# Kernel optimization log

Measured on AMD Instinct MI355X. Metric: run time of the kernel, lower is better.

## Reference

```python
import jax, jax.numpy as jnp
import numpy as np

N_NODES = 50000
N_EDGES = 1_600_000
IN_DIM = 128
HID = 32
HEADS = 4
NEG_SLOPE = 0.2


def setup_inputs() -> dict:
    key = jax.random.key(0)
    ks = jax.random.split(key, 6)
    h = jax.random.normal(ks[0], (N_NODES, IN_DIM), dtype=jnp.float32)
    src = jax.random.randint(ks[1], (N_EDGES,), 0, N_NODES, dtype=jnp.int32)
    dst = jax.random.randint(ks[2], (N_EDGES,), 0, N_NODES, dtype=jnp.int32)
    s = 1.0 / np.sqrt(IN_DIM)  # ~ Linear default init scale
    Wq = (jax.random.normal(ks[3], (HEADS, IN_DIM, HID), dtype=jnp.float32) * s)
    Wk = (jax.random.normal(ks[4], (HEADS, IN_DIM, HID), dtype=jnp.float32) * s)
    Wv = (jax.random.normal(ks[5], (HEADS, IN_DIM, HID), dtype=jnp.float32) * s)
    return {"h": h, "src": src, "dst": dst, "Wq": Wq, "Wk": Wk, "Wv": Wv}


def _gat_forward(h, src, dst, Wq, Wk, Wv):
    n = h.shape[0]
    # per-head projections: [H, N, D]
    q = jnp.einsum('ni,hio->hno', h, Wq)
    k = jnp.einsum('ni,hio->hno', h, Wk)
    v = jnp.einsum('ni,hio->hno', h, Wv)
    # edge scores: e = leaky_relu(<q_src, k_dst>)  -> [H, E]
    e = jax.nn.leaky_relu(jnp.einsum('hed,hed->he', q[:, src], k[:, dst]),
                          negative_slope=NEG_SLOPE)
    # segment softmax over incoming edges of each dst node
    seg_max = jax.vmap(lambda x: jax.ops.segment_max(x, dst, num_segments=n))(e)
    seg_max = jax.lax.stop_gradient(jnp.where(jnp.isfinite(seg_max), seg_max, 0.0))
    ex = jnp.exp(e - seg_max[:, dst])                       # [H, E]
    denom = jax.vmap(lambda x: jax.ops.segment_sum(x, dst, num_segments=n))(ex)
    alpha = ex / jnp.maximum(denom, 1e-9)[:, dst]           # [H, E]
    # weighted scatter-sum of source values into dst nodes: [H, N, D]
    msg = alpha[..., None] * v[:, src]
    out = jax.vmap(lambda m: jax.ops.segment_sum(m, dst, num_segments=n))(msg)
    # concat heads along feature dim -> [N, H*D]
    return out.transpose(1, 0, 2).reshape(n, HEADS * HID)


def reference(h, src, dst, Wq, Wk, Wv):
    return _gat_forward(h, src, dst, Wq, Wk, Wv)
```

## Files before the change

### kernel.cpp

```cpp
#include <hip/hip_runtime.h>
#include <hip/hip_fp16.h>

#define IN_DIM 128
#define HID 32
#define HEADS 4
#define OUTC (HEADS*HID)
#define NEG_SLOPE 0.2f
#define BSH 4
#define BN 16
#define BCAP 768
#define NBMAX 3200
#define NCOLS 384
#define WPB 192
#define NP 25
#define PSH 11
#define PCAP 72704
#define PBLK 18

typedef _Float16 f16x8 __attribute__((ext_vector_type(8)));
typedef float    f32x4 __attribute__((ext_vector_type(4)));

__device__ __forceinline__ unsigned short f2h(float f) {
    return __half_as_ushort(__float2half_rn(f));
}
__device__ __forceinline__ float2 h2f2(unsigned u) {
    __half2 h = *reinterpret_cast<__half2*>(&u);
    return __half22float2(h);
}
__device__ __forceinline__ float qdot2(const uint2& w, const float4& kd) {
    float2 a = h2f2(w.x);
    float2 b = h2f2(w.y);
    return a.x * kd.x + a.y * kd.y + b.x * kd.z + b.y * kd.w;
}
__device__ __forceinline__ void vacc2(const uint2& w, float e, float4& acc) {
    float2 a = h2f2(w.x);
    float2 b = h2f2(w.y);
    acc.x = fmaf(e, a.x, acc.x);
    acc.y = fmaf(e, a.y, acc.y);
    acc.z = fmaf(e, b.x, acc.z);
    acc.w = fmaf(e, b.y, acc.w);
}

__global__ __launch_bounds__(256) void w_prep(
    const float* __restrict__ Wq, const float* __restrict__ Wk,
    const float* __restrict__ Wv, unsigned short* __restrict__ Wt,
    int* __restrict__ gcount, int* __restrict__ pcount)
{
    int idx = blockIdx.x * 256 + threadIdx.x;
    if (idx < NBMAX) gcount[idx] = 0;
    if (idx >= NBMAX && idx < NBMAX + NP) pcount[idx - NBMAX] = 0;
    if (idx >= NCOLS * IN_DIM) return;
    int c = idx >> 7, k = idx & 127;
    int sel = c >> 7;
    int cc  = c & 127;
    int head = cc >> 5, dcol = cc & 31;
    const float* W = (sel == 0) ? Wk : (sel == 1) ? Wq : Wv;
    Wt[idx] = f2h(W[(size_t)head * IN_DIM * HID + (size_t)k * HID + dcol]);
}

__global__ __launch_bounds__(256) void part_proj(
    const int* __restrict__ src, const int* __restrict__ dst,
    int* __restrict__ pcount, unsigned* __restrict__ ppairs,
    const float* __restrict__ h, const unsigned short* __restrict__ Wt,
    unsigned short* __restrict__ K, unsigned short* __restrict__ Qa,
    unsigned short* __restrict__ Va,
    int ne, int binblk, int n)
{
    __shared__ __align__(16) char smem_raw[32 * IN_DIM * 2];
    const int tid = threadIdx.x;

    if ((int)blockIdx.x < binblk) {
        int* hist = (int*)smem_raw;
        int* base = hist + 32;
        const int bblk = blockIdx.x;

        if (tid < 32) hist[tid] = 0;
        __syncthreads();

        const int ne4 = ne >> 2;
        const int4* s4 = (const int4*)src;
        const int4* d4 = (const int4*)dst;

        int4 sv[4], dv[4];
        int loc[16], pk[16];
        bool val[4];
#pragma unroll
        for (int k2 = 0; k2 < 4; ++k2) {
            int idx = bblk * 1024 + k2 * 256 + tid;
            val[k2] = idx < ne4;
            if (val[k2]) { sv[k2] = s4[idx]; dv[k2] = d4[idx]; }
            else { sv[k2] = make_int4(0,0,0,0); dv[k2] = make_int4(0,0,0,0); }
        }
#pragma unroll
        for (int k2 = 0; k2 < 4; ++k2) {
            int dd[4] = { dv[k2].x, dv[k2].y, dv[k2].z, dv[k2].w };
#pragma unroll
            for (int j = 0; j < 4; ++j) {
                int p = dd[j] >> PSH;
                pk[k2*4+j]  = p;
                loc[k2*4+j] = val[k2] ? atomicAdd(&hist[p], 1) : 0;
            }
        }
        __syncthreads();
        if (tid < 32) base[tid] = hist[tid] ? atomicAdd(&pcount[tid], hist[tid]) : 0;
        __syncthreads();
#pragma unroll
        for (int k2 = 0; k2 < 4; ++k2) {
            if (!val[k2]) continue;
            int ss[4] = { sv[k2].x, sv[k2].y, sv[k2].z, sv[k2].w };
            int dd[4] = { dv[k2].x, dv[k2].y, dv[k2].z, dv[k2].w };
#pragma unroll
            for (int j = 0; j < 4; ++j) {
                int p   = pk[k2*4+j];
                int pos = base[p] + loc[k2*4+j];
                if (pos < PCAP)
                    ppairs[(size_t)p * PCAP + pos] =
                        ((unsigned)ss[j] << 16) | (unsigned)dd[j];
            }
        }
        if (bblk == 0 && tid == 0) {
            for (int e = ne4 * 4; e < ne; ++e) {
                int p   = dst[e] >> PSH;
                int pos = atomicAdd(&pcount[p], 1);
                if (pos < PCAP)
                    ppairs[(size_t)p * PCAP + pos] =
                        ((unsigned)src[e] << 16) | (unsigned)dst[e];
            }
        }
        return;
    }

    unsigned short* hsm = (unsigned short*)smem_raw;
    const int row0 = (blockIdx.x - binblk) * 32;

    for (int idx = tid; idx < 32 * 64; idx += 256) {
        int r  = idx >> 6;
        int c2 = idx & 63;
        int gr = row0 + r;
        float2 hv = (gr < n) ? ((const float2*)h)[(size_t)gr * 64 + c2]
                             : make_float2(0.f, 0.f);
        int col = c2 * 2;
        int sc  = col ^ ((r & 7) << 3);
        __half2 packed = __floats2half2_rn(hv.x, hv.y);
        *(unsigned*)&hsm[r * IN_DIM + sc] = *(unsigned*)&packed;
    }
    __syncthreads();

    const int w = tid >> 6;
    const int l = tid & 63;
    const int l15 = l & 15;
    const int kg  = l >> 4;
    const _Float16* Wt16 = (const _Float16*)Wt;

    f32x4 acc[2][6];
#pragma unroll
    for (int rt = 0; rt < 2; ++rt)
#pragma unroll
        for (int ct = 0; ct < 6; ++ct) acc[rt][ct] = (f32x4){0.f, 0.f, 0.f, 0.f};

#pragma unroll
    for (int s = 0; s < 4; ++s) {
        int scol = (s * 32 + kg * 8) ^ ((l & 7) << 3);
        f16x8 a0 = *(const f16x8*)&hsm[l15 * IN_DIM + scol];
        f16x8 a1 = *(const f16x8*)&hsm[(l15 + 16) * IN_DIM + scol];
#pragma unroll
        for (int ct = 0; ct < 6; ++ct) {
            int c = w * 96 + ct * 16 + l15;
            f16x8 b = *(const f16x8*)&Wt16[(size_t)c * IN_DIM + s * 32 + kg * 8];
            acc[0][ct] = __builtin_amdgcn_mfma_f32_16x16x32_f16(a0, b, acc[0][ct], 0, 0, 0);
            acc[1][ct] = __builtin_amdgcn_mfma_f32_16x16x32_f16(a1, b, acc[1][ct], 0, 0, 0);
        }
    }

#pragma unroll
    for (int rt = 0; rt < 2; ++rt) {
#pragma unroll
        for (int ct = 0; ct < 6; ++ct) {
            int cD = w * 96 + ct * 16 + l15;
#pragma unroll
            for (int r = 0; r < 4; ++r) {
                int node = row0 + rt * 16 + kg * 4 + r;
                if (node >= n) continue;
                unsigned short hv = f2h(acc[rt][ct][r]);
                if (cD < 128) {
                    K[(size_t)node * OUTC + cD] = hv;
                } else if (cD < 256) {
                    Qa[(size_t)node * OUTC + (cD - 128)] = hv;
                } else {
                    Va[(size_t)node * OUTC + (cD - 256)] = hv;
                }
            }
        }
    }
}

__global__ __launch_bounds__(256) void pass2(
    const unsigned* __restrict__ ppairs, const int* __restrict__ pcount,
    int* __restrict__ gcount, unsigned* __restrict__ pairs)
{
    __shared__ int hist[128], base[128];
    const int p   = blockIdx.x / PBLK;
    const int c   = blockIdx.x % PBLK;
    const int tid = threadIdx.x;

    int mp = pcount[p]; if (mp > PCAP) mp = PCAP;
    const int i0 = c * 4096;
    if (i0 >= mp) return;
    const int iend = min(i0 + 4096, mp);

    if (tid < 128) hist[tid] = 0;
    __syncthreads();

    const unsigned* pp = ppairs + (size_t)p * PCAP;
    unsigned rec[16];
    int loc[16], lb[16];
#pragma unroll
    for (int k = 0; k < 16; ++k) {
        int i = i0 + k * 256 + tid;
        if (i < iend) {
            unsigned r = pp[i];
            rec[k] = r;
            int b = ((r & 0xFFFFu) >> BSH) & 127;
            lb[k]  = b;
            loc[k] = atomicAdd(&hist[b], 1);
        } else {
            rec[k] = 0; lb[k] = -1; loc[k] = 0;
        }
    }
    __syncthreads();
    if (tid < 128) base[tid] = hist[tid] ? atomicAdd(&gcount[p * 128 + tid], hist[tid]) : 0;
    __syncthreads();
#pragma unroll
    for (int k = 0; k < 16; ++k) {
        if (lb[k] < 0) continue;
        unsigned r = rec[k];
        int gb  = p * 128 + lb[k];
        int pos = base[lb[k]] + loc[k];
        if (pos < BCAP)
            pairs[(size_t)gb * BCAP + pos] =
                ((r >> 16) << BSH) | (r & (BN - 1));
    }
}

__global__ __launch_bounds__(256) void gat_bucket(
    const unsigned* __restrict__ pairs, const int* __restrict__ gcount,
    const uint2* __restrict__ Q2, const uint2* __restrict__ V2,
    const ushort4* __restrict__ K4,
    float* __restrict__ out, int n, int nbuck)
{
    __shared__ unsigned short sl[BCAP];
    __shared__ float exls[BCAP * 4];
    __shared__ int cl[BN], cur[BN], off[BN + 1];

    const int b = blockIdx.x;
    if (b >= nbuck) return;
    const int tid = threadIdx.x;

    if (tid < BN) cl[tid] = 0;
    __syncthreads();

    int m = gcount[b]; if (m > BCAP) m = BCAP;
    const unsigned* pb = pairs + (size_t)b * BCAP;

    for (int i = tid; i < m; i += 256) atomicAdd(&cl[pb[i] & (BN - 1)], 1);
    __syncthreads();
    if (tid == 0) {
        int a = 0;
#pragma unroll
        for (int i = 0; i < BN; ++i) { off[i] = a; cur[i] = a; a += cl[i]; }
        off[BN] = a;
    }
    __syncthreads();
    for (int i = tid; i < m; i += 256) {
        unsigned p = pb[i];
        int pos = atomicAdd(&cur[p & (BN - 1)], 1);
        sl[pos] = (unsigned short)(p >> BSH);
    }
    __syncthreads();

    const int gi   = tid >> 5;
    const int l32  = tid & 31;
    const int hsel = l32 >> 3;
    const bool wr  = (l32 & 7) == 0;

    float dsum[BN / 8];

#pragma unroll
    for (int q = 0; q < BN / 8; ++q) {
        int nl   = q * 8 + gi;
        int node = b * BN + nl;
        float ds = 0.f;
        if (node < n) {
            ushort4 kh = K4[(size_t)node * 32 + l32];
            float2 k01 = h2f2(*(unsigned*)&kh.x);
            float2 k23 = h2f2(*(unsigned*)&kh.z);
            const float4 kd = make_float4(k01.x, k01.y, k23.x, k23.y);

            int j        = off[nl];
            const int je = off[nl + 1];
            for (; j + 3 < je; j += 4) {
                int s0 = sl[j], s1 = sl[j + 1], s2 = sl[j + 2], s3 = sl[j + 3];
                uint2 w0 = Q2[(size_t)s0 * 32 + l32];
                uint2 w1 = Q2[(size_t)s1 * 32 + l32];
                uint2 w2 = Q2[(size_t)s2 * 32 + l32];
                uint2 w3 = Q2[(size_t)s3 * 32 + l32];
                float p0 = qdot2(w0, kd), p1 = qdot2(w1, kd);
                float p2 = qdot2(w2, kd), p3 = qdot2(w3, kd);
#pragma unroll
                for (int o = 1; o < 8; o <<= 1) {
                    p0 += __shfl_xor(p0, o, 8);
                    p1 += __shfl_xor(p1, o, 8);
                    p2 += __shfl_xor(p2, o, 8);
                    p3 += __shfl_xor(p3, o, 8);
                }
                float e0 = __expf(p0 > 0.f ? p0 : NEG_SLOPE * p0);
                float e1 = __expf(p1 > 0.f ? p1 : NEG_SLOPE * p1);
                float e2 = __expf(p2 > 0.f ? p2 : NEG_SLOPE * p2);
                float e3 = __expf(p3 > 0.f ? p3 : NEG_SLOPE * p3);
                ds += (e0 + e1) + (e2 + e3);
                if (wr) {
                    exls[(j    ) * 4 + hsel] = e0;
                    exls[(j + 1) * 4 + hsel] = e1;
                    exls[(j + 2) * 4 + hsel] = e2;
                    exls[(j + 3) * 4 + hsel] = e3;
                }
            }
            for (; j < je; ++j) {
                int s0 = sl[j];
                uint2 w0 = Q2[(size_t)s0 * 32 + l32];
                float p0 = qdot2(w0, kd);
#pragma unroll
                for (int o = 1; o < 8; o <<= 1) p0 += __shfl_xor(p0, o, 8);
                float e0 = __expf(p0 > 0.f ? p0 : NEG_SLOPE * p0);
                ds += e0;
                if (wr) exls[j * 4 + hsel] = e0;
            }
        }
        dsum[q] = ds;
    }
    __syncthreads();

#pragma unroll
    for (int q = 0; q < BN / 8; ++q) {
        int nl   = q * 8 + gi;
        int node = b * BN + nl;
        if (node >= n) continue;

        int j        = off[nl];
        const int je = off[nl + 1];
        float4 acc = make_float4(0.f, 0.f, 0.f, 0.f);

        for (; j + 3 < je; j += 4) {
            int s0 = sl[j], s1 = sl[j + 1], s2 = sl[j + 2], s3 = sl[j + 3];
            uint2 w0 = V2[(size_t)s0 * 32 + l32];
            uint2 w1 = V2[(size_t)s1 * 32 + l32];
            uint2 w2 = V2[(size_t)s2 * 32 + l32];
            uint2 w3 = V2[(size_t)s3 * 32 + l32];
            float e0 = exls[(j    ) * 4 + hsel];
            float e1 = exls[(j + 1) * 4 + hsel];
            float e2 = exls[(j + 2) * 4 + hsel];
            float e3 = exls[(j + 3) * 4 + hsel];
            vacc2(w0, e0, acc); vacc2(w1, e1, acc);
            vacc2(w2, e2, acc); vacc2(w3, e3, acc);
        }
        for (; j < je; ++j) {
            int s0 = sl[j];
            uint2 w0 = V2[(size_t)s0 * 32 + l32];
            float e0 = exls[j * 4 + hsel];
            vacc2(w0, e0, acc);
        }

        float inv = 1.f / fmaxf(dsum[q], 1e-9f);
        float4 o; o.x = acc.x*inv; o.y = acc.y*inv; o.z = acc.z*inv; o.w = acc.w*inv;
        ((float4*)out)[(size_t)node * 32 + l32] = o;
    }
}

extern "C" void kernel_launch(void* const* d_in, const int* in_sizes, int n_in,
                              void* d_out, int out_size, void* d_ws, size_t ws_size,
                              hipStream_t stream) {
    const float* h   = (const float*)d_in[0];
    const int*   src = (const int*)d_in[1];
    const int*   dst = (const int*)d_in[2];
    const float* Wq  = (const float*)d_in[3];
    const float* Wk  = (const float*)d_in[4];
    const float* Wv  = (const float*)d_in[5];
    float* out = (float*)d_out;

    const int n     = in_sizes[0] / IN_DIM;
    const int ne    = in_sizes[1];
    const int nbuck = (n + BN - 1) >> BSH;

    unsigned short* K      = (unsigned short*)d_ws;
    unsigned short* Qa     = K  + (size_t)n * OUTC;
    unsigned short* Va     = Qa + (size_t)n * OUTC;
    int*            gcount = (int*)(Va + (size_t)n * OUTC);
    int*            pcount = gcount + NBMAX;
    unsigned*       ppairs = (unsigned*)(pcount + 64);
    unsigned*       pairs  = ppairs + (size_t)NP * PCAP;
    unsigned short* Wt     = (unsigned short*)(pairs + (size_t)NBMAX * BCAP);

    w_prep<<<WPB, 256, 0, stream>>>(Wq, Wk, Wv, Wt, gcount, pcount);

    int ne4     = ne >> 2;
    int binblk  = (ne4 + 1023) / 1024;
    int projblk = (n + 31) / 32;
    part_proj<<<binblk + projblk, 256, 0, stream>>>(
        src, dst, pcount, ppairs, h, Wt, K, Qa, Va, ne, binblk, n);

    pass2<<<NP * PBLK, 256, 0, stream>>>(ppairs, pcount, gcount, pairs);

    gat_bucket<<<nbuck, 256, 0, stream>>>(pairs, gcount, (const uint2*)Qa,
                                          (const uint2*)Va, (const ushort4*)K,
                                          out, n, nbuck);
}
```

Measured before the change: 171.0 us.

## Regroup kernel stages so weight prep overlaps partitioning and projection overlaps pass2

Weight conversion now runs in the same launch as the first partition pass. The second binning pass shares a launch with the MFMA projection, which used to run alongside the first pass. Counter zeroing moves to a hipMemsetAsync, and the partition histogram is split per wavefront to reduce LDS atomic contention. Projection output is staged through padded shared memory so K/Q/V are written with wide coalesced stores, and h is loaded as float4. The stated aim is to cut one kernel launch and the serialization between stages, at the cost of extra global atomics and a larger shared-memory footprint in the projection blocks.

```diff
diff --git a/kernel.cpp b/kernel.cpp
--- a/kernel.cpp
+++ b/kernel.cpp
@@ -16,6 +16,7 @@
 #define PSH 11
 #define PCAP 72704
 #define PBLK 18
+#define OSTRIDE 392
 
 typedef _Float16 f16x8 __attribute__((ext_vector_type(8)));
 typedef float    f32x4 __attribute__((ext_vector_type(4)));
@@ -41,108 +42,162 @@
     acc.w = fmaf(e, b.y, acc.w);
 }
 
-__global__ __launch_bounds__(256) void w_prep(
+__global__ __launch_bounds__(256) void kA_prep_part(
     const float* __restrict__ Wq, const float* __restrict__ Wk,
     const float* __restrict__ Wv, unsigned short* __restrict__ Wt,
-    int* __restrict__ gcount, int* __restrict__ pcount)
+    int* __restrict__ pcount,
+    const int* __restrict__ src, const int* __restrict__ dst,
+    unsigned* __restrict__ ppairs, int ne)
 {
-    int idx = blockIdx.x * 256 + threadIdx.x;
-    if (idx < NBMAX) gcount[idx] = 0;
-    if (idx >= NBMAX && idx < NBMAX + NP) pcount[idx - NBMAX] = 0;
-    if (idx >= NCOLS * IN_DIM) return;
-    int c = idx >> 7, k = idx & 127;
-    int sel = c >> 7;
-    int cc  = c & 127;
-    int head = cc >> 5, dcol = cc & 31;
-    const float* W = (sel == 0) ? Wk : (sel == 1) ? Wq : Wv;
-    Wt[idx] = f2h(W[(size_t)head * IN_DIM * HID + (size_t)k * HID + dcol]);
-}
-
-__global__ __launch_bounds__(256) void part_proj(
-    const int* __restrict__ src, const int* __restrict__ dst,
-    int* __restrict__ pcount, unsigned* __restrict__ ppairs,
+    const int tid = threadIdx.x;
+
+    if ((int)blockIdx.x < WPB) {
+        int idx = blockIdx.x * 256 + tid;
+        if (idx >= NCOLS * IN_DIM) return;
+        int c = idx >> 7, k = idx & 127;
+        int sel = c >> 7;
+        int cc  = c & 127;
+        int head = cc >> 5, dcol = cc & 31;
+        const float* W = (sel == 0) ? Wk : (sel == 1) ? Wq : Wv;
+        Wt[idx] = f2h(W[(size_t)head * IN_DIM * HID + (size_t)k * HID + dcol]);
+        return;
+    }
+
+    __shared__ int hist[4 * 32];
+    __shared__ int base[4 * 32];
+    const int bblk = blockIdx.x - WPB;
+    const int wid  = tid >> 6;
+
+    if (tid < 128) hist[tid] = 0;
+    __syncthreads();
+
+    const int ne4 = ne >> 2;
+    const int4* s4 = (const int4*)src;
+    const int4* d4 = (const int4*)dst;
+
+    int4 sv[4], dv[4];
+    int loc[16], pk[16];
+    bool val[4];
+#pragma unroll
+    for (int k2 = 0; k2 < 4; ++k2) {
+        int idx = bblk * 1024 + k2 * 256 + tid;
+        val[k2] = idx < ne4;
+        if (val[k2]) { sv[k2] = s4[idx]; dv[k2] = d4[idx]; }
+        else { sv[k2] = make_int4(0,0,0,0); dv[k2] = make_int4(0,0,0,0); }
+    }
+#pragma unroll
+    for (int k2 = 0; k2 < 4; ++k2) {
+        int dd[4] = { dv[k2].x, dv[k2].y, dv[k2].z, dv[k2].w };
+#pragma unroll
+        for (int j = 0; j < 4; ++j) {
+            int p = dd[j] >> PSH;
+            pk[k2*4+j]  = p;
+            loc[k2*4+j] = val[k2] ? atomicAdd(&hist[wid * 32 + p], 1) : 0;
+        }
+    }
+    __syncthreads();
+    if (tid < 128)
+        base[tid] = hist[tid] ? atomicAdd(&pcount[tid & 31], hist[tid]) : 0;
+    __syncthreads();
+#pragma unroll
+    for (int k2 = 0; k2 < 4; ++k2) {
+        if (!val[k2]) continue;
+        int ss[4] = { sv[k2].x, sv[k2].y, sv[k2].z, sv[k2].w };
+        int dd[4] = { dv[k2].x, dv[k2].y, dv[k2].z, dv[k2].w };
+#pragma unroll
+        for (int j = 0; j < 4; ++j) {
+            int p   = pk[k2*4+j];
+            int pos = base[wid * 32 + p] + loc[k2*4+j];
+            if (pos >= 0 && pos < PCAP)
+                ppairs[(size_t)p * PCAP + pos] =
+                    ((unsigned)ss[j] << 16) | (unsigned)dd[j];
+        }
+    }
+    if (bblk == 0 && tid == 0) {
+        for (int e = ne4 * 4; e < ne; ++e) {
+            int p   = dst[e] >> PSH;
+            int pos = atomicAdd(&pcount[p], 1);
+            if (pos >= 0 && pos < PCAP)
+                ppairs[(size_t)p * PCAP + pos] =
+                    ((unsigned)src[e] << 16) | (unsigned)dst[e];
+        }
+    }
+}
+
+__global__ __launch_bounds__(256) void kB_bin_proj(
+    const unsigned* __restrict__ ppairs, const int* __restrict__ pcount,
+    int* __restrict__ gcount, unsigned* __restrict__ pairs,
     const float* __restrict__ h, const unsigned short* __restrict__ Wt,
     unsigned short* __restrict__ K, unsigned short* __restrict__ Qa,
     unsigned short* __restrict__ Va,
-    int ne, int binblk, int n)
+    int p2blk, int n)
 {
-    __shared__ __align__(16) char smem_raw[32 * IN_DIM * 2];
+    __shared__ __align__(16) char smem_raw[32 * OSTRIDE * 2];
     const int tid = threadIdx.x;
 
-    if ((int)blockIdx.x < binblk) {
+    if ((int)blockIdx.x < p2blk) {
         int* hist = (int*)smem_raw;
-        int* base = hist + 32;
-        const int bblk = blockIdx.x;
-
-        if (tid < 32) hist[tid] = 0;
+        int* base = hist + 128;
+        const int p = blockIdx.x / PBLK;
+        const int c = blockIdx.x % PBLK;
+
+        int mp = pcount[p]; if (mp > PCAP) mp = PCAP;
+        const int i0 = c * 4096;
+        if (i0 >= mp) return;
+        const int iend = min(i0 + 4096, mp);
+
+        if (tid < 128) hist[tid] = 0;
         __syncthreads();
 
-        const int ne4 = ne >> 2;
-        const int4* s4 = (const int4*)src;
-        const int4* d4 = (const int4*)dst;
-
-        int4 sv[4], dv[4];
-        int loc[16], pk[16];
-        bool val[4];
-#pragma unroll
-        for (int k2 = 0; k2 < 4; ++k2) {
-            int idx = bblk * 1024 + k2 * 256 + tid;
-            val[k2] = idx < ne4;
-            if (val[k2]) { sv[k2] = s4[idx]; dv[k2] = d4[idx]; }
-            else { sv[k2] = make_int4(0,0,0,0); dv[k2] = make_int4(0,0,0,0); }
-        }
-#pragma unroll
-        for (int k2 = 0; k2 < 4; ++k2) {
-            int dd[4] = { dv[k2].x, dv[k2].y, dv[k2].z, dv[k2].w };
-#pragma unroll
-            for (int j = 0; j < 4; ++j) {
-                int p = dd[j] >> PSH;
-                pk[k2*4+j]  = p;
-                loc[k2*4+j] = val[k2] ? atomicAdd(&hist[p], 1) : 0;
+        const unsigned* pp = ppairs + (size_t)p * PCAP;
+        unsigned rec[16];
+        int loc[16], lb[16];
+#pragma unroll
+        for (int k = 0; k < 16; ++k) {
+            int i = i0 + k * 256 + tid;
+            if (i < iend) {
+                unsigned r = pp[i];
+                rec[k] = r;
+                int b = ((r & 0xFFFFu) >> BSH) & 127;
+                lb[k]  = b;
+                loc[k] = atomicAdd(&hist[b], 1);
+            } else {
+                rec[k] = 0; lb[k] = -1; loc[k] = 0;
             }
         }
         __syncthreads();
-        if (tid < 32) base[tid] = hist[tid] ? atomicAdd(&pcount[tid], hist[tid]) : 0;
+        if (tid < 128)
+            base[tid] = hist[tid] ? atomicAdd(&gcount[p * 128 + tid], hist[tid]) : 0;
         __syncthreads();
 #pragma unroll
-        for (int k2 = 0; k2 < 4; ++k2) {
-            if (!val[k2]) continue;
-            int ss[4] = { sv[k2].x, sv[k2].y, sv[k2].z, sv[k2].w };
-            int dd[4] = { dv[k2].x, dv[k2].y, dv[k2].z, dv[k2].w };
-#pragma unroll
-            for (int j = 0; j < 4; ++j) {
-                int p   = pk[k2*4+j];
-                int pos = base[p] + loc[k2*4+j];
-                if (pos < PCAP)
-                    ppairs[(size_t)p * PCAP + pos] =
-                        ((unsigned)ss[j] << 16) | (unsigned)dd[j];
-            }
-        }
-        if (bblk == 0 && tid == 0) {
-            for (int e = ne4 * 4; e < ne; ++e) {
-                int p   = dst[e] >> PSH;
-                int pos = atomicAdd(&pcount[p], 1);
-                if (pos < PCAP)
-                    ppairs[(size_t)p * PCAP + pos] =
-                        ((unsigned)src[e] << 16) | (unsigned)dst[e];
-            }
+        for (int k = 0; k < 16; ++k) {
+            if (lb[k] < 0) continue;
+            unsigned r = rec[k];
+            int gb  = p * 128 + lb[k];
+            int pos = base[lb[k]] + loc[k];
+            if (pos < BCAP)
+                pairs[(size_t)gb * BCAP + pos] =
+                    ((r >> 16) << BSH) | (r & (BN - 1));
         }
         return;
     }
 
     unsigned short* hsm = (unsigned short*)smem_raw;
-    const int row0 = (blockIdx.x - binblk) * 32;
-
-    for (int idx = tid; idx < 32 * 64; idx += 256) {
-        int r  = idx >> 6;
-        int c2 = idx & 63;
+    const int row0 = (blockIdx.x - p2blk) * 32;
+
+    for (int idx = tid; idx < 32 * 32; idx += 256) {
+        int r  = idx >> 5;
+        int c4 = idx & 31;
         int gr = row0 + r;
-        float2 hv = (gr < n) ? ((const float2*)h)[(size_t)gr * 64 + c2]
-                             : make_float2(0.f, 0.f);
-        int col = c2 * 2;
-        int sc  = col ^ ((r & 7) << 3);
-        __half2 packed = __floats2half2_rn(hv.x, hv.y);
-        *(unsigned*)&hsm[r * IN_DIM + sc] = *(unsigned*)&packed;
+        float4 hv = (gr < n) ? ((const float4*)h)[(size_t)gr * 32 + c4]
+                             : make_float4(0.f, 0.f, 0.f, 0.f);
+        int sc = (c4 * 4) ^ ((r & 7) << 3);
+        __half2 p01 = __floats2half2_rn(hv.x, hv.y);
+        __half2 p23 = __floats2half2_rn(hv.z, hv.w);
+        uint2 u;
+        u.x = *(unsigned*)&p01;
+        u.y = *(unsigned*)&p23;
+        *(uint2*)&hsm[r * IN_DIM + sc] = u;
     }
     __syncthreads();
 
@@ -171,7 +226,9 @@
             acc[1][ct] = __builtin_amdgcn_mfma_f32_16x16x32_f16(a1, b, acc[1][ct], 0, 0, 0);
         }
     }
-
+    __syncthreads();
+
+    unsigned short* osm = (unsigned short*)smem_raw;
 #pragma unroll
     for (int rt = 0; rt < 2; ++rt) {
 #pragma unroll
@@ -179,66 +236,26 @@
             int cD = w * 96 + ct * 16 + l15;
 #pragma unroll
             for (int r = 0; r < 4; ++r) {
-                int node = row0 + rt * 16 + kg * 4 + r;
-                if (node >= n) continue;
-                unsigned short hv = f2h(acc[rt][ct][r]);
-                if (cD < 128) {
-                    K[(size_t)node * OUTC + cD] = hv;
-                } else if (cD < 256) {
-                    Qa[(size_t)node * OUTC + (cD - 128)] = hv;
-                } else {
-                    Va[(size_t)node * OUTC + (cD - 256)] = hv;
-                }
+                int rowl = rt * 16 + kg * 4 + r;
+                osm[rowl * OSTRIDE + cD] = f2h(acc[rt][ct][r]);
             }
         }
     }
-}
-
-__global__ __launch_bounds__(256) void pass2(
-    const unsigned* __restrict__ ppairs, const int* __restrict__ pcount,
-    int* __restrict__ gcount, unsigned* __restrict__ pairs)
-{
-    __shared__ int hist[128], base[128];
-    const int p   = blockIdx.x / PBLK;
-    const int c   = blockIdx.x % PBLK;
-    const int tid = threadIdx.x;
-
-    int mp = pcount[p]; if (mp > PCAP) mp = PCAP;
-    const int i0 = c * 4096;
-    if (i0 >= mp) return;
-    const int iend = min(i0 + 4096, mp);
-
-    if (tid < 128) hist[tid] = 0;
-    __syncthreads();
-
-    const unsigned* pp = ppairs + (size_t)p * PCAP;
-    unsigned rec[16];
-    int loc[16], lb[16];
-#pragma unroll
-    for (int k = 0; k < 16; ++k) {
-        int i = i0 + k * 256 + tid;
-        if (i < iend) {
-            unsigned r = pp[i];
-            rec[k] = r;
-            int b = ((r & 0xFFFFu) >> BSH) & 127;
-            lb[k]  = b;
-            loc[k] = atomicAdd(&hist[b], 1);
-        } else {
-            rec[k] = 0; lb[k] = -1; loc[k] = 0;
-        }
-    }
-    __syncthreads();
-    if (tid < 128) base[tid] = hist[tid] ? atomicAdd(&gcount[p * 128 + tid], hist[tid]) : 0;
-    __syncthreads();
-#pragma unroll
-    for (int k = 0; k < 16; ++k) {
-        if (lb[k] < 0) continue;
-        unsigned r = rec[k];
-        int gb  = p * 128 + lb[k];
-        int pos = base[lb[k]] + loc[k];
-        if (pos < BCAP)
-            pairs[(size_t)gb * BCAP + pos] =
-                ((r >> 16) << BSH) | (r & (BN - 1));
+    __syncthreads();
+
+    for (int c = tid; c < 32 * 96; c += 256) {
+        int row  = c / 96;
+        int col4 = c - row * 96;
+        int node = row0 + row;
+        if (node >= n) continue;
+        uint2 v = *(const uint2*)&osm[row * OSTRIDE + col4 * 4];
+        int colbase = col4 * 4;
+        if (colbase < 128)
+            *(uint2*)&K [(size_t)node * OUTC + colbase] = v;
+        else if (colbase < 256)
+            *(uint2*)&Qa[(size_t)node * OUTC + (colbase - 128)] = v;
+        else
+            *(uint2*)&Va[(size_t)node * OUTC + (colbase - 256)] = v;
     }
 }
 
@@ -400,15 +417,17 @@
     unsigned*       pairs  = ppairs + (size_t)NP * PCAP;
     unsigned short* Wt     = (unsigned short*)(pairs + (size_t)NBMAX * BCAP);
 
-    w_prep<<<WPB, 256, 0, stream>>>(Wq, Wk, Wv, Wt, gcount, pcount);
-
-    int ne4     = ne >> 2;
-    int binblk  = (ne4 + 1023) / 1024;
+    hipMemsetAsync(gcount, 0, (NBMAX + 64) * sizeof(int), stream);
+
+    int ne4    = ne >> 2;
+    int binblk = (ne4 + 1023) / 1024;
+    kA_prep_part<<<WPB + binblk, 256, 0, stream>>>(
+        Wq, Wk, Wv, Wt, pcount, src, dst, ppairs, ne);
+
+    int p2blk   = NP * PBLK;
     int projblk = (n + 31) / 32;
-    part_proj<<<binblk + projblk, 256, 0, stream>>>(
-        src, dst, pcount, ppairs, h, Wt, K, Qa, Va, ne, binblk, n);
-
-    pass2<<<NP * PBLK, 256, 0, stream>>>(ppairs, pcount, gcount, pairs);
+    kB_bin_proj<<<p2blk + projblk, 256, 0, stream>>>(
+        ppairs, pcount, gcount, pairs, h, Wt, K, Qa, Va, p2blk, n);
 
     gat_bucket<<<nbuck, 256, 0, stream>>>(pairs, gcount, (const uint2*)Qa,
                                           (const uint2*)Va, (const ushort4*)K,
```

Result: slower. 201.5 us (+17.8%).
